# Kernel tuning notes

Hardware: AMD Instinct MI355X
Metric: run time of the kernel (lower is better)

## Reference

```python
import jax, jax.numpy as jnp
import numpy as np

FACTOR = 5

def setup_inputs() -> dict:
    key = jax.random.key(0)
    k1, k2, k3, k4 = jax.random.split(key, 4)
    B, L, H, D = 4, 4096, 8, 64
    sample_k = min(FACTOR * int(np.ceil(np.log(L))), L)  # 45
    queries = jax.random.normal(k1, (B, L, H, D), jnp.float32)
    keys = jax.random.normal(k2, (B, L, H, D), jnp.float32)
    values = jax.random.normal(k3, (B, L, H, D), jnp.float32)
    # torch.randint(L_K, (L_Q, sample_k)) hoisted here for determinism
    index_sample = jax.random.randint(k4, (L, sample_k), 0, L, dtype=jnp.int32)
    return {"queries": queries, "keys": keys, "values": values,
            "index_sample": index_sample}


def reference(queries, keys, values, index_sample):
    B, L_Q, H, D = queries.shape
    L_K = keys.shape[1]
    # [B,L,H,D] -> [B,H,L,D]
    Q = jnp.transpose(queries, (0, 2, 1, 3))
    K = jnp.transpose(keys, (0, 2, 1, 3))
    V = jnp.transpose(values, (0, 2, 1, 3))

    u = min(FACTOR * int(np.ceil(np.log(L_Q))), L_Q)  # n_top queries

    # --- _prob_QK: sampled QK, sparsity measure, top-u query selection ---
    # K_sample[b,h,q,s,:] = K[b,h,index_sample[q,s],:]
    K_sample = K[:, :, index_sample, :]                        # [B,H,L_Q,Sk,D]
    Q_K_sample = jnp.einsum('bhqd,bhqsd->bhqs', Q, K_sample)   # [B,H,L_Q,Sk]
    M = Q_K_sample.max(axis=-1) - Q_K_sample.sum(axis=-1) / L_K
    _, M_top = jax.lax.top_k(M, u)                             # [B,H,u]

    Q_reduce = jnp.take_along_axis(Q, M_top[..., None], axis=2)  # [B,H,u,D]
    scale = 1.0 / np.sqrt(D).astype(np.float32)
    scores = jnp.einsum('bhud,bhkd->bhuk', Q_reduce, K) * scale  # [B,H,u,L_K]

    # --- masked causal attention on the selected rows (mask_flag=True) ---
    # ProbMask: triu(1) rows gathered at M_top -> mask where col > query pos
    causal_mask = M_top[..., None] < jnp.arange(L_K)             # [B,H,u,L_K]
    scores = jnp.where(causal_mask, -jnp.inf, scores)
    attn = jax.nn.softmax(scores, axis=-1)

    # --- initial context (masked => cumsum of V), scatter top-u updates ---
    context = jnp.cumsum(V, axis=2)                              # [B,H,L_Q,D]
    update = jnp.einsum('bhuk,bhkd->bhud', attn, V)              # [B,H,u,D]
    b_idx = jnp.arange(B)[:, None, None]
    h_idx = jnp.arange(H)[None, :, None]
    context = context.at[b_idx, h_idx, M_top].set(update)
    return context  # [B,H,L_Q,D]
```

## Files before the change

kernel.cpp:

```cpp
#include <hip/hip_runtime.h>
#include <float.h>
#include <math.h>

#define B_ 4
#define L_ 4096
#define H_ 8
#define D_ 64
#define S_ 45
#define KC_ 16
#define KCH_ 256
#define SCALE 0.125f

typedef __attribute__((ext_vector_type(8))) short short8;
typedef __attribute__((ext_vector_type(4))) float float4v;

__device__ __forceinline__ ushort f2bf(float x) {
  unsigned u = __float_as_uint(x);
  return (ushort)((u + 0x7FFFu + ((u >> 16) & 1u)) >> 16);
}

__device__ __forceinline__ int swz_us(int row, int col_b, int rowb, int m) {
  int slot = (col_b >> 4) ^ (row & m);
  return row * (rowb >> 1) + (slot << 3) + ((col_b & 15) >> 1);
}

__global__ __launch_bounds__(256) void kA(
    const float* __restrict__ Q, const float* __restrict__ K,
    const float* __restrict__ V, const int* __restrict__ idxs,
    float* __restrict__ M, float* __restrict__ cs)
{
  int blk = blockIdx.x;
  int grp = blk / 136, within = blk % 136;
  int tid = threadIdx.x;
  int w = tid >> 6, lane = tid & 63;

  if (within >= 128) {
    if (grp >= 64) return;
    int cblk = grp * 8 + (within - 128);
    int bh = cblk >> 4, cg = cblk & 15;
    int b = bh >> 3, h = bh & 7;
    int t = lane & 15, rg = lane >> 4;
    int c = cg * 4 + w;
    int l0 = c * 64;
    const float4* V4 = (const float4*)V;
    float4 acc = make_float4(0.f, 0.f, 0.f, 0.f);
    for (int step = 0; step < 16; ++step) {
      int l = l0 + step * 4 + rg;
      float4 v = V4[((size_t)(b * L_ + l) * H_ + h) * 16 + t];
      acc.x += v.x; acc.y += v.y; acc.z += v.z; acc.w += v.w;
    }
    acc.x += __shfl_xor(acc.x, 16, 64); acc.y += __shfl_xor(acc.y, 16, 64);
    acc.z += __shfl_xor(acc.z, 16, 64); acc.w += __shfl_xor(acc.w, 16, 64);
    acc.x += __shfl_xor(acc.x, 32, 64); acc.y += __shfl_xor(acc.y, 32, 64);
    acc.z += __shfl_xor(acc.z, 32, 64); acc.w += __shfl_xor(acc.w, 32, 64);
    if (rg == 0)
      ((float4*)cs)[((size_t)bh * 64 + c) * 16 + t] = acc;
    return;
  }

  int kblk = grp * 128 + within;
  int phase = kblk >> 13;
  int pblk = kblk & 8191;
  int g = pblk & 7;
  int b = (g >> 2) + phase * 2;
  int hq = g & 3;
  int chunk = pblk >> 3;
  int l = chunk * 4 + w;
  int t31 = lane & 31;
  int half = lane >> 5;

  const float4* qp =
      (const float4*)(Q + ((size_t)(b * L_ + l) * H_ + hq * 2) * D_);
  float4 qv = qp[t31];

  int s = lane < S_ ? lane : S_ - 1;
  int idxall = idxs[l * S_ + s];

  float vmax = -FLT_MAX, vsum = 0.f;
  #pragma unroll
  for (int c = 0; c < 3; ++c) {
    int kidx[6];
    #pragma unroll
    for (int jj = 0; jj < 6; ++jj)
      kidx[jj] = __shfl(idxall, (c * 6 + jj) * 2 + half, 64);
    float4 kv[6];
    #pragma unroll
    for (int jj = 0; jj < 6; ++jj)
      kv[jj] = ((const float4*)(K +
          ((size_t)(b * L_ + kidx[jj]) * H_ + hq * 2) * D_))[t31];
    #pragma unroll
    for (int jj = 0; jj < 6; ++jj) {
      float p = qv.x * kv[jj].x;
      p = fmaf(qv.y, kv[jj].y, p);
      p = fmaf(qv.z, kv[jj].z, p);
      p = fmaf(qv.w, kv[jj].w, p);
      p += __shfl_xor(p, 1, 64);
      p += __shfl_xor(p, 2, 64);
      p += __shfl_xor(p, 4, 64);
      p += __shfl_xor(p, 8, 64);
      vmax = fmaxf(vmax, p);
      vsum += p;
    }
  }
  {
    int kidx[5];
    #pragma unroll
    for (int jj = 0; jj < 5; ++jj) {
      int s2 = (18 + jj) * 2 + half;
      kidx[jj] = __shfl(idxall, s2 > 44 ? 44 : s2, 64);
    }
    float4 kv[5];
    #pragma unroll
    for (int jj = 0; jj < 5; ++jj)
      kv[jj] = ((const float4*)(K +
          ((size_t)(b * L_ + kidx[jj]) * H_ + hq * 2) * D_))[t31];
    #pragma unroll
    for (int jj = 0; jj < 5; ++jj) {
      float p = qv.x * kv[jj].x;
      p = fmaf(qv.y, kv[jj].y, p);
      p = fmaf(qv.z, kv[jj].z, p);
      p = fmaf(qv.w, kv[jj].w, p);
      p += __shfl_xor(p, 1, 64);
      p += __shfl_xor(p, 2, 64);
      p += __shfl_xor(p, 4, 64);
      p += __shfl_xor(p, 8, 64);
      bool dup = (jj == 4) && (half == 1);
      vmax = fmaxf(vmax, p);
      if (!dup) vsum += p;
    }
  }
  vmax = fmaxf(vmax, __shfl_xor(vmax, 32, 64));
  vsum += __shfl_xor(vsum, 32, 64);
  if ((lane & 15) == 0 && half == 0) {
    int h = hq * 2 + (lane >> 4);
    M[(size_t)(b * H_ + h) * L_ + l] = vmax - vsum * (1.0f / L_);
  }
}

__device__ __forceinline__ unsigned ordf(float f) {
  unsigned u = __float_as_uint(f);
  return (u & 0x80000000u) ? ~u : (u | 0x80000000u);
}

__global__ __launch_bounds__(256) void kB(
    const float* __restrict__ M, int* __restrict__ mtop, float* __restrict__ cs)
{
  int blk = blockIdx.x;
  int tid = threadIdx.x;
  if (blk >= 32) {
    int g = (blk - 32) * 256 + tid;
    int bh = g >> 6, d = g & 63;
    float v[64];
    #pragma unroll
    for (int c = 0; c < 64; ++c) v[c] = cs[((size_t)bh * 64 + c) * D_ + d];
    float run = 0.f;
    #pragma unroll
    for (int c = 0; c < 64; ++c) {
      float a = v[c];
      cs[((size_t)bh * 64 + c) * D_ + d] = run;
      run += a;
    }
    return;
  }
  __shared__ unsigned long long cand[4][S_];
  int bh = blk;
  int w = tid >> 6, lane = tid & 63;
  const float* Mp = M + (size_t)bh * L_;
  unsigned long long key[16];
  #pragma unroll
  for (int j = 0; j < 16; ++j) {
    int gi = w * 1024 + j * 64 + lane;
    key[j] = ((unsigned long long)ordf(Mp[gi]) << 32) | (unsigned)(~gi);
  }
  for (int it = 0; it < S_; ++it) {
    unsigned long long loc = key[0];
    #pragma unroll
    for (int j = 1; j < 16; ++j) loc = key[j] > loc ? key[j] : loc;
    unsigned long long best = loc;
    #pragma unroll
    for (int m = 32; m >= 1; m >>= 1) {
      unsigned long long o = __shfl_xor(best, m, 64);
      best = o > best ? o : best;
    }
    if (loc == best) {
      #pragma unroll
      for (int j = 0; j < 16; ++j) if (key[j] == best) key[j] = 0ull;
    }
    if (lane == 0) cand[w][it] = best;
  }
  __syncthreads();
  if (w == 0) {
    unsigned long long k2[3];
    #pragma unroll
    for (int j = 0; j < 3; ++j) {
      int c = j * 64 + lane;
      k2[j] = (c < 4 * S_) ? cand[c / S_][c % S_] : 0ull;
    }
    for (int it = 0; it < S_; ++it) {
      unsigned long long loc = k2[0];
      loc = k2[1] > loc ? k2[1] : loc;
      loc = k2[2] > loc ? k2[2] : loc;
      unsigned long long best = loc;
      #pragma unroll
      for (int m = 32; m >= 1; m >>= 1) {
        unsigned long long o = __shfl_xor(best, m, 64);
        best = o > best ? o : best;
      }
      if (loc == best) {
        #pragma unroll
        for (int j = 0; j < 3; ++j) if (k2[j] == best) k2[j] = 0ull;
      }
      if (lane == 0) mtop[bh * S_ + it] = (int)(~(unsigned)(best & 0xFFFFFFFFu));
    }
  }
}

__global__ __launch_bounds__(256) void kATT(
    const float* __restrict__ Q, const float* __restrict__ K,
    const float* __restrict__ V, const int* __restrict__ mtop,
    float* __restrict__ lpart, float* __restrict__ updp)
{
  __shared__ __align__(16) ushort Ks[256 * 64];
  __shared__ __align__(16) ushort Qs[48 * 64];
  __shared__ __align__(16) ushort Ps[48 * 256];
  __shared__ float lred[4][48];
  __shared__ int   cut[48];

  int blk = blockIdx.x;
  int kc = blk >> 5;
  int r5 = blk & 31;
  int bh = ((r5 & 7) << 2) | (r5 >> 3);
  int b = bh >> 3, h = bh & 7;
  int tid = threadIdx.x;
  int w = tid >> 6, lane = tid & 63;
  int l15 = lane & 15, l4 = lane >> 4;

  if (tid < 48) cut[tid] = (tid < S_) ? mtop[bh * S_ + tid] : -1;
  __syncthreads();

  {
    const float4* kp =
        (const float4*)(K + ((size_t)(b * L_ + kc * KCH_ + tid) * H_ + h) * D_);
    #pragma unroll
    for (int c = 0; c < 8; ++c) {
      float4 a = kp[2 * c], bb = kp[2 * c + 1];
      uint4 pk;
      pk.x = f2bf(a.x) | ((unsigned)f2bf(a.y) << 16);
      pk.y = f2bf(a.z) | ((unsigned)f2bf(a.w) << 16);
      pk.z = f2bf(bb.x) | ((unsigned)f2bf(bb.y) << 16);
      pk.w = f2bf(bb.z) | ((unsigned)f2bf(bb.w) << 16);
      *(uint4*)&Ks[swz_us(tid, c * 16, 128, 7)] = pk;
    }
  }
  for (int i = tid; i < 48 * 8; i += 256) {
    int row = i >> 3, c = i & 7;
    uint4 pk = make_uint4(0, 0, 0, 0);
    if (row < S_) {
      const float4* qp =
          (const float4*)(Q + ((size_t)(b * L_ + cut[row]) * H_ + h) * D_);
      float4 a = qp[2 * c], bb = qp[2 * c + 1];
      pk.x = f2bf(a.x) | ((unsigned)f2bf(a.y) << 16);
      pk.y = f2bf(a.z) | ((unsigned)f2bf(a.w) << 16);
      pk.z = f2bf(bb.x) | ((unsigned)f2bf(bb.y) << 16);
      pk.w = f2bf(bb.z) | ((unsigned)f2bf(bb.w) << 16);
    }
    *(uint4*)&Qs[swz_us(row, c * 16, 128, 7)] = pk;
  }
  __syncthreads();

  float4v accS[3][4];
  #pragma unroll
  for (int mt = 0; mt < 3; ++mt)
    #pragma unroll
    for (int nt = 0; nt < 4; ++nt)
      accS[mt][nt] = (float4v){0.f, 0.f, 0.f, 0.f};
  #pragma unroll
  for (int ks = 0; ks < 2; ++ks) {
    short8 afr[3];
    #pragma unroll
    for (int mt = 0; mt < 3; ++mt)
      afr[mt] = *(const short8*)&Qs[swz_us(mt * 16 + l15, ks * 64 + l4 * 16, 128, 7)];
    #pragma unroll
    for (int nt = 0; nt < 4; ++nt) {
      short8 bfr = *(const short8*)
          &Ks[swz_us(w * 64 + nt * 16 + l15, ks * 64 + l4 * 16, 128, 7)];
      #pragma unroll
      for (int mt = 0; mt < 3; ++mt)
        accS[mt][nt] = __builtin_amdgcn_mfma_f32_16x16x32_bf16(
            afr[mt], bfr, accS[mt][nt], 0, 0, 0);
    }
  }

  #pragma unroll
  for (int mt = 0; mt < 3; ++mt) {
    #pragma unroll
    for (int j = 0; j < 4; ++j) {
      int row = mt * 16 + l4 * 4 + j;
      int ct = cut[row];
      float rs = 0.f;
      #pragma unroll
      for (int nt = 0; nt < 4; ++nt) {
        int col = w * 64 + nt * 16 + l15;
        int kg = kc * KCH_ + col;
        float e = (kg <= ct) ? __expf(accS[mt][nt][j] * SCALE) : 0.f;
        rs += e;
        Ps[swz_us(row, col * 2, 512, 15)] = f2bf(e);
      }
      rs += __shfl_xor(rs, 1, 64);
      rs += __shfl_xor(rs, 2, 64);
      rs += __shfl_xor(rs, 4, 64);
      rs += __shfl_xor(rs, 8, 64);
      if (l15 == 0) lred[w][row] = rs;
    }
  }
  __syncthreads();

  if (tid < S_)
    lpart[((size_t)(bh * KC_ + kc)) * S_ + tid] =
        lred[0][tid] + lred[1][tid] + lred[2][tid] + lred[3][tid];

  {
    const float4* vp =
        (const float4*)(V + ((size_t)(b * L_ + kc * KCH_ + tid) * H_ + h) * D_);
    #pragma unroll
    for (int c = 0; c < 16; ++c) {
      float4 v = vp[c];
      int d0 = c * 4;
      Ks[swz_us(d0 + 0, tid * 2, 512, 15)] = f2bf(v.x);
      Ks[swz_us(d0 + 1, tid * 2, 512, 15)] = f2bf(v.y);
      Ks[swz_us(d0 + 2, tid * 2, 512, 15)] = f2bf(v.z);
      Ks[swz_us(d0 + 3, tid * 2, 512, 15)] = f2bf(v.w);
    }
  }
  __syncthreads();

  float4v accU[3];
  #pragma unroll
  for (int i = 0; i < 3; ++i) accU[i] = (float4v){0.f, 0.f, 0.f, 0.f};
  #pragma unroll
  for (int ks = 0; ks < 8; ++ks) {
    #pragma unroll
    for (int i = 0; i < 3; ++i) {
      int pi = w * 3 + i, mt = pi >> 2, nt = pi & 3;
      short8 afr = *(const short8*)
          &Ps[swz_us(mt * 16 + l15, ks * 64 + l4 * 16, 512, 15)];
      short8 bfr = *(const short8*)
          &Ks[swz_us(nt * 16 + l15, ks * 64 + l4 * 16, 512, 15)];
      accU[i] = __builtin_amdgcn_mfma_f32_16x16x32_bf16(afr, bfr, accU[i], 0, 0, 0);
    }
  }
  float* up = updp + ((size_t)(bh * KC_ + kc)) * (S_ * D_);
  #pragma unroll
  for (int i = 0; i < 3; ++i) {
    int pi = w * 3 + i, mt = pi >> 2, nt = pi & 3;
    #pragma unroll
    for (int j = 0; j < 4; ++j) {
      int row = mt * 16 + l4 * 4 + j;
      if (row < S_) up[row * D_ + nt * 16 + l15] = accU[i][j];
    }
  }
}

__global__ __launch_bounds__(256) void kWD(
    const float* __restrict__ V, const float* __restrict__ cs,
    const float* __restrict__ lpart, const float* __restrict__ updp,
    const int* __restrict__ mtop, float* __restrict__ out)
{
  int blk = blockIdx.x;
  int tid = threadIdx.x;

  if (blk >= 512) {
    __shared__ float linv[S_];
    __shared__ int   mt[S_];
    int bh = blk - 512;
    if (tid < S_) {
      float l = 0.f;
      for (int kc = 0; kc < KC_; ++kc) l += lpart[(size_t)(bh * KC_ + kc) * S_ + tid];
      linv[tid] = 1.0f / l;
      mt[tid] = mtop[bh * S_ + tid];
    }
    __syncthreads();
    for (int i = tid; i < S_ * D_; i += 256) {
      int r = i >> 6, d = i & 63;
      float u = 0.f;
      for (int kc = 0; kc < KC_; ++kc)
        u += updp[((size_t)(bh * KC_ + kc)) * (S_ * D_) + i];
      out[((size_t)bh * L_ + mt[r]) * D_ + d] = u * linv[r];
    }
    return;
  }

  __shared__ unsigned bits[8];
  int bh = blk >> 4, cg = blk & 15;
  int base = cg * 256;
  if (tid < 8) bits[tid] = 0u;
  __syncthreads();
  if (tid < S_) {
    int r = mtop[bh * S_ + tid] - base;
    if ((unsigned)r < 256u) atomicOr(&bits[r >> 5], 1u << (r & 31));
  }
  __syncthreads();

  int b = bh >> 3, h = bh & 7;
  int w = tid >> 6, lane = tid & 63;
  int t = lane & 15, rg = lane >> 4;
  int c = cg * 4 + w;
  int l0 = c * 64;
  const float4* V4 = (const float4*)V;
  float4* O4 = (float4*)out;
  float4 carry = ((const float4*)cs)[((size_t)bh * 64 + c) * 16 + t];
  for (int step = 0; step < 16; ++step) {
    int l = l0 + step * 4 + rg;
    float4 v = V4[((size_t)(b * L_ + l) * H_ + h) * 16 + t];
    float4 u;
    u.x = __shfl_up(v.x, 16, 64); u.y = __shfl_up(v.y, 16, 64);
    u.z = __shfl_up(v.z, 16, 64); u.w = __shfl_up(v.w, 16, 64);
    if (rg >= 1) { v.x += u.x; v.y += u.y; v.z += u.z; v.w += u.w; }
    u.x = __shfl_up(v.x, 32, 64); u.y = __shfl_up(v.y, 32, 64);
    u.z = __shfl_up(v.z, 32, 64); u.w = __shfl_up(v.w, 32, 64);
    if (rg >= 2) { v.x += u.x; v.y += u.y; v.z += u.z; v.w += u.w; }
    int wl = l - base;
    if (!((bits[wl >> 5] >> (wl & 31)) & 1u)) {
      float4 o;
      o.x = carry.x + v.x; o.y = carry.y + v.y;
      o.z = carry.z + v.z; o.w = carry.w + v.w;
      O4[((size_t)bh * L_ + l) * 16 + t] = o;
    }
    carry.x += __shfl(v.x, 48 + t, 64); carry.y += __shfl(v.y, 48 + t, 64);
    carry.z += __shfl(v.z, 48 + t, 64); carry.w += __shfl(v.w, 48 + t, 64);
  }
}

extern "C" void kernel_launch(void* const* d_in, const int* in_sizes, int n_in,
                              void* d_out, int out_size, void* d_ws, size_t ws_size,
                              hipStream_t stream) {
  const float* Q = (const float*)d_in[0];
  const float* K = (const float*)d_in[1];
  const float* V = (const float*)d_in[2];
  const int*   I = (const int*)d_in[3];
  float* out = (float*)d_out;
  float* ws = (float*)d_ws;

  float* M     = ws;
  float* cs    = ws + 131072;
  float* lpart = ws + 262144;
  float* updp  = ws + 262144 + 23040;
  int*   mtop  = (int*)(ws + 262144 + 23040 + 1474560);

  kA<<<128 * 136, 256, 0, stream>>>(Q, K, V, I, M, cs);
  kB<<<40, 256, 0, stream>>>(M, mtop, cs);
  kATT<<<B_ * H_ * KC_, 256, 0, stream>>>(Q, K, V, mtop, lpart, updp);
  kWD<<<544, 256, 0, stream>>>(V, cs, lpart, updp, mtop, out);
}
```

Measured before the change: 174.9 us.

## Merge top-k, attention and writeback into one cooperative kernel with grid syncs

New measurement: 380.4 us. 117% more time.

```diff
diff --git a/kernel.cpp b/kernel.cpp
--- a/kernel.cpp
+++ b/kernel.cpp
@@ -1,6 +1,9 @@
 #include <hip/hip_runtime.h>
+#include <hip/hip_cooperative_groups.h>
 #include <float.h>
 #include <math.h>
+
+namespace cg = cooperative_groups;
 
 #define B_ 4
 #define L_ 4096
@@ -22,6 +25,11 @@
 __device__ __forceinline__ int swz_us(int row, int col_b, int rowb, int m) {
   int slot = (col_b >> 4) ^ (row & m);
   return row * (rowb >> 1) + (slot << 3) + ((col_b & 15) >> 1);
+}
+
+__device__ __forceinline__ unsigned ordf(float f) {
+  unsigned u = __float_as_uint(f);
+  return (u & 0x80000000u) ? ~u : (u | 0x80000000u);
 }
 
 __global__ __launch_bounds__(256) void kA(
@@ -137,88 +145,12 @@
   }
 }
 
-__device__ __forceinline__ unsigned ordf(float f) {
-  unsigned u = __float_as_uint(f);
-  return (u & 0x80000000u) ? ~u : (u | 0x80000000u);
-}
-
-__global__ __launch_bounds__(256) void kB(
-    const float* __restrict__ M, int* __restrict__ mtop, float* __restrict__ cs)
-{
-  int blk = blockIdx.x;
-  int tid = threadIdx.x;
-  if (blk >= 32) {
-    int g = (blk - 32) * 256 + tid;
-    int bh = g >> 6, d = g & 63;
-    float v[64];
-    #pragma unroll
-    for (int c = 0; c < 64; ++c) v[c] = cs[((size_t)bh * 64 + c) * D_ + d];
-    float run = 0.f;
-    #pragma unroll
-    for (int c = 0; c < 64; ++c) {
-      float a = v[c];
-      cs[((size_t)bh * 64 + c) * D_ + d] = run;
-      run += a;
-    }
-    return;
-  }
-  __shared__ unsigned long long cand[4][S_];
-  int bh = blk;
-  int w = tid >> 6, lane = tid & 63;
-  const float* Mp = M + (size_t)bh * L_;
-  unsigned long long key[16];
-  #pragma unroll
-  for (int j = 0; j < 16; ++j) {
-    int gi = w * 1024 + j * 64 + lane;
-    key[j] = ((unsigned long long)ordf(Mp[gi]) << 32) | (unsigned)(~gi);
-  }
-  for (int it = 0; it < S_; ++it) {
-    unsigned long long loc = key[0];
-    #pragma unroll
-    for (int j = 1; j < 16; ++j) loc = key[j] > loc ? key[j] : loc;
-    unsigned long long best = loc;
-    #pragma unroll
-    for (int m = 32; m >= 1; m >>= 1) {
-      unsigned long long o = __shfl_xor(best, m, 64);
-      best = o > best ? o : best;
-    }
-    if (loc == best) {
-      #pragma unroll
-      for (int j = 0; j < 16; ++j) if (key[j] == best) key[j] = 0ull;
-    }
-    if (lane == 0) cand[w][it] = best;
-  }
-  __syncthreads();
-  if (w == 0) {
-    unsigned long long k2[3];
-    #pragma unroll
-    for (int j = 0; j < 3; ++j) {
-      int c = j * 64 + lane;
-      k2[j] = (c < 4 * S_) ? cand[c / S_][c % S_] : 0ull;
-    }
-    for (int it = 0; it < S_; ++it) {
-      unsigned long long loc = k2[0];
-      loc = k2[1] > loc ? k2[1] : loc;
-      loc = k2[2] > loc ? k2[2] : loc;
-      unsigned long long best = loc;
-      #pragma unroll
-      for (int m = 32; m >= 1; m >>= 1) {
-        unsigned long long o = __shfl_xor(best, m, 64);
-        best = o > best ? o : best;
-      }
-      if (loc == best) {
-        #pragma unroll
-        for (int j = 0; j < 3; ++j) if (k2[j] == best) k2[j] = 0ull;
-      }
-      if (lane == 0) mtop[bh * S_ + it] = (int)(~(unsigned)(best & 0xFFFFFFFFu));
-    }
-  }
-}
-
-__global__ __launch_bounds__(256) void kATT(
+__global__ __launch_bounds__(256) void kT(
     const float* __restrict__ Q, const float* __restrict__ K,
-    const float* __restrict__ V, const int* __restrict__ mtop,
-    float* __restrict__ lpart, float* __restrict__ updp)
+    const float* __restrict__ V, const float* __restrict__ M,
+    float* __restrict__ cs, int* __restrict__ mtop,
+    float* __restrict__ lpart, float* __restrict__ updp,
+    float* __restrict__ out, int phase)
 {
   __shared__ __align__(16) ushort Ks[256 * 64];
   __shared__ __align__(16) ushort Qs[48 * 64];
@@ -227,207 +159,286 @@
   __shared__ int   cut[48];
 
   int blk = blockIdx.x;
+  int tid = threadIdx.x;
+  int w = tid >> 6, lane = tid & 63;
+  bool coop = (phase == 0);
+
   int kc = blk >> 5;
   int r5 = blk & 31;
-  int bh = ((r5 & 7) << 2) | (r5 >> 3);
-  int b = bh >> 3, h = bh & 7;
-  int tid = threadIdx.x;
-  int w = tid >> 6, lane = tid & 63;
-  int l15 = lane & 15, l4 = lane >> 4;
-
-  if (tid < 48) cut[tid] = (tid < S_) ? mtop[bh * S_ + tid] : -1;
-  __syncthreads();
-
-  {
-    const float4* kp =
-        (const float4*)(K + ((size_t)(b * L_ + kc * KCH_ + tid) * H_ + h) * D_);
-    #pragma unroll
-    for (int c = 0; c < 8; ++c) {
-      float4 a = kp[2 * c], bb = kp[2 * c + 1];
-      uint4 pk;
-      pk.x = f2bf(a.x) | ((unsigned)f2bf(a.y) << 16);
-      pk.y = f2bf(a.z) | ((unsigned)f2bf(a.w) << 16);
-      pk.z = f2bf(bb.x) | ((unsigned)f2bf(bb.y) << 16);
-      pk.w = f2bf(bb.z) | ((unsigned)f2bf(bb.w) << 16);
-      *(uint4*)&Ks[swz_us(tid, c * 16, 128, 7)] = pk;
-    }
-  }
-  for (int i = tid; i < 48 * 8; i += 256) {
-    int row = i >> 3, c = i & 7;
-    uint4 pk = make_uint4(0, 0, 0, 0);
-    if (row < S_) {
-      const float4* qp =
-          (const float4*)(Q + ((size_t)(b * L_ + cut[row]) * H_ + h) * D_);
-      float4 a = qp[2 * c], bb = qp[2 * c + 1];
-      pk.x = f2bf(a.x) | ((unsigned)f2bf(a.y) << 16);
-      pk.y = f2bf(a.z) | ((unsigned)f2bf(a.w) << 16);
-      pk.z = f2bf(bb.x) | ((unsigned)f2bf(bb.y) << 16);
-      pk.w = f2bf(bb.z) | ((unsigned)f2bf(bb.w) << 16);
-    }
-    *(uint4*)&Qs[swz_us(row, c * 16, 128, 7)] = pk;
-  }
-  __syncthreads();
-
-  float4v accS[3][4];
-  #pragma unroll
-  for (int mt = 0; mt < 3; ++mt)
-    #pragma unroll
-    for (int nt = 0; nt < 4; ++nt)
-      accS[mt][nt] = (float4v){0.f, 0.f, 0.f, 0.f};
-  #pragma unroll
-  for (int ks = 0; ks < 2; ++ks) {
-    short8 afr[3];
+  int bh_att = ((r5 & 7) << 2) | (r5 >> 3);
+  int b_att = bh_att >> 3, h_att = bh_att & 7;
+
+  if (coop || phase == 1) {
+    if (blk < 32) {
+      unsigned long long (*cand)[S_] = (unsigned long long (*)[S_])Ps;
+      int bh = blk;
+      const float* Mp = M + (size_t)bh * L_;
+      unsigned long long key[16];
+      #pragma unroll
+      for (int j = 0; j < 16; ++j) {
+        int gi = w * 1024 + j * 64 + lane;
+        key[j] = ((unsigned long long)ordf(Mp[gi]) << 32) | (unsigned)(~gi);
+      }
+      for (int it = 0; it < S_; ++it) {
+        unsigned long long loc = key[0];
+        #pragma unroll
+        for (int j = 1; j < 16; ++j) loc = key[j] > loc ? key[j] : loc;
+        unsigned long long best = loc;
+        #pragma unroll
+        for (int m = 32; m >= 1; m >>= 1) {
+          unsigned long long o = __shfl_xor(best, m, 64);
+          best = o > best ? o : best;
+        }
+        if (loc == best) {
+          #pragma unroll
+          for (int j = 0; j < 16; ++j) if (key[j] == best) key[j] = 0ull;
+        }
+        if (lane == 0) cand[w][it] = best;
+      }
+      __syncthreads();
+      if (w == 0) {
+        unsigned long long k2[3];
+        #pragma unroll
+        for (int j = 0; j < 3; ++j) {
+          int c = j * 64 + lane;
+          k2[j] = (c < 4 * S_) ? cand[c / S_][c % S_] : 0ull;
+        }
+        for (int it = 0; it < S_; ++it) {
+          unsigned long long loc = k2[0];
+          loc = k2[1] > loc ? k2[1] : loc;
+          loc = k2[2] > loc ? k2[2] : loc;
+          unsigned long long best = loc;
+          #pragma unroll
+          for (int m = 32; m >= 1; m >>= 1) {
+            unsigned long long o = __shfl_xor(best, m, 64);
+            best = o > best ? o : best;
+          }
+          if (loc == best) {
+            #pragma unroll
+            for (int j = 0; j < 3; ++j) if (k2[j] == best) k2[j] = 0ull;
+          }
+          if (lane == 0) mtop[bh * S_ + it] = (int)(~(unsigned)(best & 0xFFFFFFFFu));
+        }
+      }
+    } else if (blk < 40) {
+      int g = (blk - 32) * 256 + tid;
+      int bh = g >> 6, d = g & 63;
+      float v[64];
+      #pragma unroll
+      for (int c = 0; c < 64; ++c) v[c] = cs[((size_t)bh * 64 + c) * D_ + d];
+      float run = 0.f;
+      #pragma unroll
+      for (int c = 0; c < 64; ++c) {
+        float a = v[c];
+        cs[((size_t)bh * 64 + c) * D_ + d] = run;
+        run += a;
+      }
+    } else if (coop) {
+      const float4* kp =
+          (const float4*)(K + ((size_t)(b_att * L_ + kc * KCH_ + tid) * H_ + h_att) * D_);
+      #pragma unroll
+      for (int c = 0; c < 8; ++c) {
+        float4 a = kp[2 * c], bb = kp[2 * c + 1];
+        uint4 pk;
+        pk.x = f2bf(a.x) | ((unsigned)f2bf(a.y) << 16);
+        pk.y = f2bf(a.z) | ((unsigned)f2bf(a.w) << 16);
+        pk.z = f2bf(bb.x) | ((unsigned)f2bf(bb.y) << 16);
+        pk.w = f2bf(bb.z) | ((unsigned)f2bf(bb.w) << 16);
+        *(uint4*)&Ks[swz_us(tid, c * 16, 128, 7)] = pk;
+      }
+    }
+  }
+  if (coop) { __threadfence(); cg::this_grid().sync(); }
+
+  if (coop || phase == 2) {
+    if (!coop || blk < 40) {
+      const float4* kp =
+          (const float4*)(K + ((size_t)(b_att * L_ + kc * KCH_ + tid) * H_ + h_att) * D_);
+      #pragma unroll
+      for (int c = 0; c < 8; ++c) {
+        float4 a = kp[2 * c], bb = kp[2 * c + 1];
+        uint4 pk;
+        pk.x = f2bf(a.x) | ((unsigned)f2bf(a.y) << 16);
+        pk.y = f2bf(a.z) | ((unsigned)f2bf(a.w) << 16);
+        pk.z = f2bf(bb.x) | ((unsigned)f2bf(bb.y) << 16);
+        pk.w = f2bf(bb.z) | ((unsigned)f2bf(bb.w) << 16);
+        *(uint4*)&Ks[swz_us(tid, c * 16, 128, 7)] = pk;
+      }
+    }
+    if (tid < 48) cut[tid] = (tid < S_) ? mtop[bh_att * S_ + tid] : -1;
+    __syncthreads();
+    for (int i = tid; i < 48 * 8; i += 256) {
+      int row = i >> 3, c = i & 7;
+      uint4 pk = make_uint4(0, 0, 0, 0);
+      if (row < S_) {
+        const float4* qp =
+            (const float4*)(Q + ((size_t)(b_att * L_ + cut[row]) * H_ + h_att) * D_);
+        float4 a = qp[2 * c], bb = qp[2 * c + 1];
+        pk.x = f2bf(a.x) | ((unsigned)f2bf(a.y) << 16);
+        pk.y = f2bf(a.z) | ((unsigned)f2bf(a.w) << 16);
+        pk.z = f2bf(bb.x) | ((unsigned)f2bf(bb.y) << 16);
+        pk.w = f2bf(bb.z) | ((unsigned)f2bf(bb.w) << 16);
+      }
+      *(uint4*)&Qs[swz_us(row, c * 16, 128, 7)] = pk;
+    }
+    __syncthreads();
+
+    int l15 = lane & 15, l4 = lane >> 4;
+    float4v accS[3][4];
     #pragma unroll
     for (int mt = 0; mt < 3; ++mt)
-      afr[mt] = *(const short8*)&Qs[swz_us(mt * 16 + l15, ks * 64 + l4 * 16, 128, 7)];
-    #pragma unroll
-    for (int nt = 0; nt < 4; ++nt) {
-      short8 bfr = *(const short8*)
-          &Ks[swz_us(w * 64 + nt * 16 + l15, ks * 64 + l4 * 16, 128, 7)];
+      #pragma unroll
+      for (int nt = 0; nt < 4; ++nt)
+        accS[mt][nt] = (float4v){0.f, 0.f, 0.f, 0.f};
+    #pragma unroll
+    for (int ks = 0; ks < 2; ++ks) {
+      short8 afr[3];
       #pragma unroll
       for (int mt = 0; mt < 3; ++mt)
-        accS[mt][nt] = __builtin_amdgcn_mfma_f32_16x16x32_bf16(
-            afr[mt], bfr, accS[mt][nt], 0, 0, 0);
-    }
-  }
-
-  #pragma unroll
-  for (int mt = 0; mt < 3; ++mt) {
-    #pragma unroll
-    for (int j = 0; j < 4; ++j) {
-      int row = mt * 16 + l4 * 4 + j;
-      int ct = cut[row];
-      float rs = 0.f;
+        afr[mt] = *(const short8*)&Qs[swz_us(mt * 16 + l15, ks * 64 + l4 * 16, 128, 7)];
       #pragma unroll
       for (int nt = 0; nt < 4; ++nt) {
-        int col = w * 64 + nt * 16 + l15;
-        int kg = kc * KCH_ + col;
-        float e = (kg <= ct) ? __expf(accS[mt][nt][j] * SCALE) : 0.f;
-        rs += e;
-        Ps[swz_us(row, col * 2, 512, 15)] = f2bf(e);
-      }
-      rs += __shfl_xor(rs, 1, 64);
-      rs += __shfl_xor(rs, 2, 64);
-      rs += __shfl_xor(rs, 4, 64);
-      rs += __shfl_xor(rs, 8, 64);
-      if (l15 == 0) lred[w][row] = rs;
-    }
-  }
-  __syncthreads();
-
-  if (tid < S_)
-    lpart[((size_t)(bh * KC_ + kc)) * S_ + tid] =
-        lred[0][tid] + lred[1][tid] + lred[2][tid] + lred[3][tid];
-
-  {
-    const float4* vp =
-        (const float4*)(V + ((size_t)(b * L_ + kc * KCH_ + tid) * H_ + h) * D_);
-    #pragma unroll
-    for (int c = 0; c < 16; ++c) {
-      float4 v = vp[c];
-      int d0 = c * 4;
-      Ks[swz_us(d0 + 0, tid * 2, 512, 15)] = f2bf(v.x);
-      Ks[swz_us(d0 + 1, tid * 2, 512, 15)] = f2bf(v.y);
-      Ks[swz_us(d0 + 2, tid * 2, 512, 15)] = f2bf(v.z);
-      Ks[swz_us(d0 + 3, tid * 2, 512, 15)] = f2bf(v.w);
-    }
-  }
-  __syncthreads();
-
-  float4v accU[3];
-  #pragma unroll
-  for (int i = 0; i < 3; ++i) accU[i] = (float4v){0.f, 0.f, 0.f, 0.f};
-  #pragma unroll
-  for (int ks = 0; ks < 8; ++ks) {
+        short8 bfr = *(const short8*)
+            &Ks[swz_us(w * 64 + nt * 16 + l15, ks * 64 + l4 * 16, 128, 7)];
+        #pragma unroll
+        for (int mt = 0; mt < 3; ++mt)
+          accS[mt][nt] = __builtin_amdgcn_mfma_f32_16x16x32_bf16(
+              afr[mt], bfr, accS[mt][nt], 0, 0, 0);
+      }
+    }
+
+    #pragma unroll
+    for (int mt = 0; mt < 3; ++mt) {
+      #pragma unroll
+      for (int j = 0; j < 4; ++j) {
+        int row = mt * 16 + l4 * 4 + j;
+        int ct = cut[row];
+        float rs = 0.f;
+        #pragma unroll
+        for (int nt = 0; nt < 4; ++nt) {
+          int col = w * 64 + nt * 16 + l15;
+          int kg = kc * KCH_ + col;
+          float e = (kg <= ct) ? __expf(accS[mt][nt][j] * SCALE) : 0.f;
+          rs += e;
+          Ps[swz_us(row, col * 2, 512, 15)] = f2bf(e);
+        }
+        rs += __shfl_xor(rs, 1, 64);
+        rs += __shfl_xor(rs, 2, 64);
+        rs += __shfl_xor(rs, 4, 64);
+        rs += __shfl_xor(rs, 8, 64);
+        if (l15 == 0) lred[w][row] = rs;
+      }
+    }
+    __syncthreads();
+
+    if (tid < S_)
+      lpart[((size_t)(bh_att * KC_ + kc)) * S_ + tid] =
+          lred[0][tid] + lred[1][tid] + lred[2][tid] + lred[3][tid];
+
+    {
+      const float4* vp =
+          (const float4*)(V + ((size_t)(b_att * L_ + kc * KCH_ + tid) * H_ + h_att) * D_);
+      #pragma unroll
+      for (int c = 0; c < 16; ++c) {
+        float4 v = vp[c];
+        int d0 = c * 4;
+        Ks[swz_us(d0 + 0, tid * 2, 512, 15)] = f2bf(v.x);
+        Ks[swz_us(d0 + 1, tid * 2, 512, 15)] = f2bf(v.y);
+        Ks[swz_us(d0 + 2, tid * 2, 512, 15)] = f2bf(v.z);
+        Ks[swz_us(d0 + 3, tid * 2, 512, 15)] = f2bf(v.w);
+      }
+    }
+    __syncthreads();
+
+    float4v accU[3];
+    #pragma unroll
+    for (int i = 0; i < 3; ++i) accU[i] = (float4v){0.f, 0.f, 0.f, 0.f};
+    #pragma unroll
+    for (int ks = 0; ks < 8; ++ks) {
+      #pragma unroll
+      for (int i = 0; i < 3; ++i) {
+        int pi = w * 3 + i, mt = pi >> 2, nt = pi & 3;
+        short8 afr = *(const short8*)
+            &Ps[swz_us(mt * 16 + l15, ks * 64 + l4 * 16, 512, 15)];
+        short8 bfr = *(const short8*)
+            &Ks[swz_us(nt * 16 + l15, ks * 64 + l4 * 16, 512, 15)];
+        accU[i] = __builtin_amdgcn_mfma_f32_16x16x32_bf16(afr, bfr, accU[i], 0, 0, 0);
+      }
+    }
+    float* up = updp + ((size_t)(bh_att * KC_ + kc)) * (S_ * D_);
     #pragma unroll
     for (int i = 0; i < 3; ++i) {
       int pi = w * 3 + i, mt = pi >> 2, nt = pi & 3;
-      short8 afr = *(const short8*)
-          &Ps[swz_us(mt * 16 + l15, ks * 64 + l4 * 16, 512, 15)];
-      short8 bfr = *(const short8*)
-          &Ks[swz_us(nt * 16 + l15, ks * 64 + l4 * 16, 512, 15)];
-      accU[i] = __builtin_amdgcn_mfma_f32_16x16x32_bf16(afr, bfr, accU[i], 0, 0, 0);
-    }
-  }
-  float* up = updp + ((size_t)(bh * KC_ + kc)) * (S_ * D_);
-  #pragma unroll
-  for (int i = 0; i < 3; ++i) {
-    int pi = w * 3 + i, mt = pi >> 2, nt = pi & 3;
-    #pragma unroll
-    for (int j = 0; j < 4; ++j) {
-      int row = mt * 16 + l4 * 4 + j;
-      if (row < S_) up[row * D_ + nt * 16 + l15] = accU[i][j];
-    }
-  }
-}
-
-__global__ __launch_bounds__(256) void kWD(
-    const float* __restrict__ V, const float* __restrict__ cs,
-    const float* __restrict__ lpart, const float* __restrict__ updp,
-    const int* __restrict__ mtop, float* __restrict__ out)
-{
-  int blk = blockIdx.x;
-  int tid = threadIdx.x;
-
-  if (blk >= 512) {
-    __shared__ float linv[S_];
-    __shared__ int   mt[S_];
-    int bh = blk - 512;
+      #pragma unroll
+      for (int j = 0; j < 4; ++j) {
+        int row = mt * 16 + l4 * 4 + j;
+        if (row < S_) up[row * D_ + nt * 16 + l15] = accU[i][j];
+      }
+    }
+  }
+  if (coop) { __threadfence(); cg::this_grid().sync(); }
+
+  if (coop || phase == 3) {
+    unsigned* bits = (unsigned*)cut;
+    int bh = blk >> 4, cg2 = blk & 15;
+    int base = cg2 * 256;
+    if (tid < 8) bits[tid] = 0u;
+    __syncthreads();
     if (tid < S_) {
-      float l = 0.f;
-      for (int kc = 0; kc < KC_; ++kc) l += lpart[(size_t)(bh * KC_ + kc) * S_ + tid];
-      linv[tid] = 1.0f / l;
-      mt[tid] = mtop[bh * S_ + tid];
-    }
-    __syncthreads();
-    for (int i = tid; i < S_ * D_; i += 256) {
-      int r = i >> 6, d = i & 63;
-      float u = 0.f;
-      for (int kc = 0; kc < KC_; ++kc)
-        u += updp[((size_t)(bh * KC_ + kc)) * (S_ * D_) + i];
-      out[((size_t)bh * L_ + mt[r]) * D_ + d] = u * linv[r];
-    }
-    return;
-  }
-
-  __shared__ unsigned bits[8];
-  int bh = blk >> 4, cg = blk & 15;
-  int base = cg * 256;
-  if (tid < 8) bits[tid] = 0u;
-  __syncthreads();
-  if (tid < S_) {
-    int r = mtop[bh * S_ + tid] - base;
-    if ((unsigned)r < 256u) atomicOr(&bits[r >> 5], 1u << (r & 31));
-  }
-  __syncthreads();
-
-  int b = bh >> 3, h = bh & 7;
-  int w = tid >> 6, lane = tid & 63;
-  int t = lane & 15, rg = lane >> 4;
-  int c = cg * 4 + w;
-  int l0 = c * 64;
-  const float4* V4 = (const float4*)V;
-  float4* O4 = (float4*)out;
-  float4 carry = ((const float4*)cs)[((size_t)bh * 64 + c) * 16 + t];
-  for (int step = 0; step < 16; ++step) {
-    int l = l0 + step * 4 + rg;
-    float4 v = V4[((size_t)(b * L_ + l) * H_ + h) * 16 + t];
-    float4 u;
-    u.x = __shfl_up(v.x, 16, 64); u.y = __shfl_up(v.y, 16, 64);
-    u.z = __shfl_up(v.z, 16, 64); u.w = __shfl_up(v.w, 16, 64);
-    if (rg >= 1) { v.x += u.x; v.y += u.y; v.z += u.z; v.w += u.w; }
-    u.x = __shfl_up(v.x, 32, 64); u.y = __shfl_up(v.y, 32, 64);
-    u.z = __shfl_up(v.z, 32, 64); u.w = __shfl_up(v.w, 32, 64);
-    if (rg >= 2) { v.x += u.x; v.y += u.y; v.z += u.z; v.w += u.w; }
-    int wl = l - base;
-    if (!((bits[wl >> 5] >> (wl & 31)) & 1u)) {
-      float4 o;
-      o.x = carry.x + v.x; o.y = carry.y + v.y;
-      o.z = carry.z + v.z; o.w = carry.w + v.w;
-      O4[((size_t)bh * L_ + l) * 16 + t] = o;
-    }
-    carry.x += __shfl(v.x, 48 + t, 64); carry.y += __shfl(v.y, 48 + t, 64);
-    carry.z += __shfl(v.z, 48 + t, 64); carry.w += __shfl(v.w, 48 + t, 64);
+      int r = mtop[bh * S_ + tid] - base;
+      if ((unsigned)r < 256u) atomicOr(&bits[r >> 5], 1u << (r & 31));
+    }
+    __syncthreads();
+
+    int b = bh >> 3, h = bh & 7;
+    int t = lane & 15, rg = lane >> 4;
+    int c = cg2 * 4 + w;
+    int l0 = c * 64;
+    const float4* V4 = (const float4*)V;
+    float4* O4 = (float4*)out;
+    float4 carry = ((const float4*)cs)[((size_t)bh * 64 + c) * 16 + t];
+    for (int step = 0; step < 16; ++step) {
+      int l = l0 + step * 4 + rg;
+      float4 v = V4[((size_t)(b * L_ + l) * H_ + h) * 16 + t];
+      float4 u;
+      u.x = __shfl_up(v.x, 16, 64); u.y = __shfl_up(v.y, 16, 64);
+      u.z = __shfl_up(v.z, 16, 64); u.w = __shfl_up(v.w, 16, 64);
+      if (rg >= 1) { v.x += u.x; v.y += u.y; v.z += u.z; v.w += u.w; }
+      u.x = __shfl_up(v.x, 32, 64); u.y = __shfl_up(v.y, 32, 64);
+      u.z = __shfl_up(v.z, 32, 64); u.w = __shfl_up(v.w, 32, 64);
+      if (rg >= 2) { v.x += u.x; v.y += u.y; v.z += u.z; v.w += u.w; }
+      int wl = l - base;
+      if (!((bits[wl >> 5] >> (wl & 31)) & 1u)) {
+        float4 o;
+        o.x = carry.x + v.x; o.y = carry.y + v.y;
+        o.z = carry.z + v.z; o.w = carry.w + v.w;
+        O4[((size_t)bh * L_ + l) * 16 + t] = o;
+      }
+      carry.x += __shfl(v.x, 48 + t, 64); carry.y += __shfl(v.y, 48 + t, 64);
+      carry.z += __shfl(v.z, 48 + t, 64); carry.w += __shfl(v.w, 48 + t, 64);
+    }
+
+    if (blk < 32) {
+      float* linv = (float*)lred;
+      int*   mt2  = (int*)(lred) + 64;
+      int bhf = blk;
+      __syncthreads();
+      if (tid < S_) {
+        float l = 0.f;
+        for (int kcc = 0; kcc < KC_; ++kcc)
+          l += lpart[(size_t)(bhf * KC_ + kcc) * S_ + tid];
+        linv[tid] = 1.0f / l;
+        mt2[tid] = mtop[bhf * S_ + tid];
+      }
+      __syncthreads();
+      for (int i = tid; i < S_ * D_; i += 256) {
+        int r = i >> 6, d = i & 63;
+        float u = 0.f;
+        for (int kcc = 0; kcc < KC_; ++kcc)
+          u += updp[((size_t)(bhf * KC_ + kcc)) * (S_ * D_) + i];
+        out[((size_t)bhf * L_ + mt2[r]) * D_ + d] = u * linv[r];
+      }
+    }
   }
 }
 
@@ -448,7 +459,17 @@
   int*   mtop  = (int*)(ws + 262144 + 23040 + 1474560);
 
   kA<<<128 * 136, 256, 0, stream>>>(Q, K, V, I, M, cs);
-  kB<<<40, 256, 0, stream>>>(M, mtop, cs);
-  kATT<<<B_ * H_ * KC_, 256, 0, stream>>>(Q, K, V, mtop, lpart, updp);
-  kWD<<<544, 256, 0, stream>>>(V, cs, lpart, updp, mtop, out);
-}
+
+  int ph0 = 0;
+  void* args[] = {(void*)&Q, (void*)&K, (void*)&V, (void*)&M, (void*)&cs,
+                  (void*)&mtop, (void*)&lpart, (void*)&updp, (void*)&out,
+                  (void*)&ph0};
+  hipError_t e = hipLaunchCooperativeKernel((void*)kT, dim3(512), dim3(256),
+                                            args, 0, stream);
+  if (e != hipSuccess) {
+    (void)hipGetLastError();
+    kT<<<40, 256, 0, stream>>>(Q, K, V, M, cs, mtop, lpart, updp, out, 1);
+    kT<<<512, 256, 0, stream>>>(Q, K, V, M, cs, mtop, lpart, updp, out, 2);
+    kT<<<512, 256, 0, stream>>>(Q, K, V, M, cs, mtop, lpart, updp, out, 3);
+  }
+}
```

## Merge cumsum writeback into attention kernel and prefetch V into registers

Applied to the files above, without the earlier changes.

Result: slower. 187.9 us (+7.4%).

```diff
diff --git a/kernel.cpp b/kernel.cpp
--- a/kernel.cpp
+++ b/kernel.cpp
@@ -22,6 +22,11 @@
 __device__ __forceinline__ int swz_us(int row, int col_b, int rowb, int m) {
   int slot = (col_b >> 4) ^ (row & m);
   return row * (rowb >> 1) + (slot << 3) + ((col_b & 15) >> 1);
+}
+
+__device__ __forceinline__ unsigned ordf(float f) {
+  unsigned u = __float_as_uint(f);
+  return (u & 0x80000000u) ? ~u : (u | 0x80000000u);
 }
 
 __global__ __launch_bounds__(256) void kA(
@@ -135,11 +140,6 @@
     int h = hq * 2 + (lane >> 4);
     M[(size_t)(b * H_ + h) * L_ + l] = vmax - vsum * (1.0f / L_);
   }
-}
-
-__device__ __forceinline__ unsigned ordf(float f) {
-  unsigned u = __float_as_uint(f);
-  return (u & 0x80000000u) ? ~u : (u | 0x80000000u);
 }
 
 __global__ __launch_bounds__(256) void kB(
@@ -215,25 +215,80 @@
   }
 }
 
-__global__ __launch_bounds__(256) void kATT(
+__global__ __launch_bounds__(256) void kAW(
     const float* __restrict__ Q, const float* __restrict__ K,
-    const float* __restrict__ V, const int* __restrict__ mtop,
-    float* __restrict__ lpart, float* __restrict__ updp)
+    const float* __restrict__ V, const float* __restrict__ cs,
+    const int* __restrict__ mtop, float* __restrict__ lpart,
+    float* __restrict__ updp, float* __restrict__ out)
 {
   __shared__ __align__(16) ushort Ks[256 * 64];
   __shared__ __align__(16) ushort Qs[48 * 64];
   __shared__ __align__(16) ushort Ps[48 * 256];
   __shared__ float lred[4][48];
   __shared__ int   cut[48];
+  __shared__ unsigned bits[8];
 
   int blk = blockIdx.x;
-  int kc = blk >> 5;
-  int r5 = blk & 31;
+  int grp = blk >> 4, within = blk & 15;
+  int tid = threadIdx.x;
+  int w = tid >> 6, lane = tid & 63;
+
+  if (within >= 8) {
+    int wblk = grp * 8 + (within - 8);
+    int bh = wblk >> 4, cg2 = wblk & 15;
+    int base = cg2 * 256;
+    if (tid < 8) bits[tid] = 0u;
+    __syncthreads();
+    if (tid < S_) {
+      int r = mtop[bh * S_ + tid] - base;
+      if ((unsigned)r < 256u) atomicOr(&bits[r >> 5], 1u << (r & 31));
+    }
+    __syncthreads();
+
+    int b = bh >> 3, h = bh & 7;
+    int t = lane & 15, rg = lane >> 4;
+    int c = cg2 * 4 + w;
+    int l0 = c * 64;
+    const float4* V4 = (const float4*)V;
+    float4* O4 = (float4*)out;
+    float4 carry = ((const float4*)cs)[((size_t)bh * 64 + c) * 16 + t];
+    for (int step = 0; step < 16; ++step) {
+      int l = l0 + step * 4 + rg;
+      float4 v = V4[((size_t)(b * L_ + l) * H_ + h) * 16 + t];
+      float4 u;
+      u.x = __shfl_up(v.x, 16, 64); u.y = __shfl_up(v.y, 16, 64);
+      u.z = __shfl_up(v.z, 16, 64); u.w = __shfl_up(v.w, 16, 64);
+      if (rg >= 1) { v.x += u.x; v.y += u.y; v.z += u.z; v.w += u.w; }
+      u.x = __shfl_up(v.x, 32, 64); u.y = __shfl_up(v.y, 32, 64);
+      u.z = __shfl_up(v.z, 32, 64); u.w = __shfl_up(v.w, 32, 64);
+      if (rg >= 2) { v.x += u.x; v.y += u.y; v.z += u.z; v.w += u.w; }
+      int wl = l - base;
+      if (!((bits[wl >> 5] >> (wl & 31)) & 1u)) {
+        float4 o;
+        o.x = carry.x + v.x; o.y = carry.y + v.y;
+        o.z = carry.z + v.z; o.w = carry.w + v.w;
+        O4[((size_t)bh * L_ + l) * 16 + t] = o;
+      }
+      carry.x += __shfl(v.x, 48 + t, 64); carry.y += __shfl(v.y, 48 + t, 64);
+      carry.z += __shfl(v.z, 48 + t, 64); carry.w += __shfl(v.w, 48 + t, 64);
+    }
+    return;
+  }
+
+  int ablk = grp * 8 + within;
+  int kc = ablk >> 5;
+  int r5 = ablk & 31;
   int bh = ((r5 & 7) << 2) | (r5 >> 3);
   int b = bh >> 3, h = bh & 7;
-  int tid = threadIdx.x;
-  int w = tid >> 6, lane = tid & 63;
   int l15 = lane & 15, l4 = lane >> 4;
+
+  float4 vreg[16];
+  {
+    const float4* vp =
+        (const float4*)(V + ((size_t)(b * L_ + kc * KCH_ + tid) * H_ + h) * D_);
+    #pragma unroll
+    for (int c = 0; c < 16; ++c) vreg[c] = vp[c];
+  }
 
   if (tid < 48) cut[tid] = (tid < S_) ? mtop[bh * S_ + tid] : -1;
   __syncthreads();
@@ -319,18 +374,14 @@
     lpart[((size_t)(bh * KC_ + kc)) * S_ + tid] =
         lred[0][tid] + lred[1][tid] + lred[2][tid] + lred[3][tid];
 
-  {
-    const float4* vp =
-        (const float4*)(V + ((size_t)(b * L_ + kc * KCH_ + tid) * H_ + h) * D_);
-    #pragma unroll
-    for (int c = 0; c < 16; ++c) {
-      float4 v = vp[c];
-      int d0 = c * 4;
-      Ks[swz_us(d0 + 0, tid * 2, 512, 15)] = f2bf(v.x);
-      Ks[swz_us(d0 + 1, tid * 2, 512, 15)] = f2bf(v.y);
-      Ks[swz_us(d0 + 2, tid * 2, 512, 15)] = f2bf(v.z);
-      Ks[swz_us(d0 + 3, tid * 2, 512, 15)] = f2bf(v.w);
-    }
+  #pragma unroll
+  for (int c = 0; c < 16; ++c) {
+    float4 v = vreg[c];
+    int d0 = c * 4;
+    Ks[swz_us(d0 + 0, tid * 2, 512, 15)] = f2bf(v.x);
+    Ks[swz_us(d0 + 1, tid * 2, 512, 15)] = f2bf(v.y);
+    Ks[swz_us(d0 + 2, tid * 2, 512, 15)] = f2bf(v.z);
+    Ks[swz_us(d0 + 3, tid * 2, 512, 15)] = f2bf(v.w);
   }
   __syncthreads();
 
@@ -361,73 +412,26 @@
   }
 }
 
-__global__ __launch_bounds__(256) void kWD(
-    const float* __restrict__ V, const float* __restrict__ cs,
+__global__ __launch_bounds__(256) void kFin(
     const float* __restrict__ lpart, const float* __restrict__ updp,
     const int* __restrict__ mtop, float* __restrict__ out)
 {
-  int blk = blockIdx.x;
+  __shared__ float linv[S_];
+  __shared__ int   mt[S_];
+  int bh = blockIdx.x;
   int tid = threadIdx.x;
-
-  if (blk >= 512) {
-    __shared__ float linv[S_];
-    __shared__ int   mt[S_];
-    int bh = blk - 512;
-    if (tid < S_) {
-      float l = 0.f;
-      for (int kc = 0; kc < KC_; ++kc) l += lpart[(size_t)(bh * KC_ + kc) * S_ + tid];
-      linv[tid] = 1.0f / l;
-      mt[tid] = mtop[bh * S_ + tid];
-    }
-    __syncthreads();
-    for (int i = tid; i < S_ * D_; i += 256) {
-      int r = i >> 6, d = i & 63;
-      float u = 0.f;
-      for (int kc = 0; kc < KC_; ++kc)
-        u += updp[((size_t)(bh * KC_ + kc)) * (S_ * D_) + i];
-      out[((size_t)bh * L_ + mt[r]) * D_ + d] = u * linv[r];
-    }
-    return;
-  }
-
-  __shared__ unsigned bits[8];
-  int bh = blk >> 4, cg = blk & 15;
-  int base = cg * 256;
-  if (tid < 8) bits[tid] = 0u;
-  __syncthreads();
   if (tid < S_) {
-    int r = mtop[bh * S_ + tid] - base;
-    if ((unsigned)r < 256u) atomicOr(&bits[r >> 5], 1u << (r & 31));
-  }
-  __syncthreads();
-
-  int b = bh >> 3, h = bh & 7;
-  int w = tid >> 6, lane = tid & 63;
-  int t = lane & 15, rg = lane >> 4;
-  int c = cg * 4 + w;
-  int l0 = c * 64;
-  const float4* V4 = (const float4*)V;
-  float4* O4 = (float4*)out;
-  float4 carry = ((const float4*)cs)[((size_t)bh * 64 + c) * 16 + t];
-  for (int step = 0; step < 16; ++step) {
-    int l = l0 + step * 4 + rg;
-    float4 v = V4[((size_t)(b * L_ + l) * H_ + h) * 16 + t];
-    float4 u;
-    u.x = __shfl_up(v.x, 16, 64); u.y = __shfl_up(v.y, 16, 64);
-    u.z = __shfl_up(v.z, 16, 64); u.w = __shfl_up(v.w, 16, 64);
-    if (rg >= 1) { v.x += u.x; v.y += u.y; v.z += u.z; v.w += u.w; }
-    u.x = __shfl_up(v.x, 32, 64); u.y = __shfl_up(v.y, 32, 64);
-    u.z = __shfl_up(v.z, 32, 64); u.w = __shfl_up(v.w, 32, 64);
-    if (rg >= 2) { v.x += u.x; v.y += u.y; v.z += u.z; v.w += u.w; }
-    int wl = l - base;
-    if (!((bits[wl >> 5] >> (wl & 31)) & 1u)) {
-      float4 o;
-      o.x = carry.x + v.x; o.y = carry.y + v.y;
-      o.z = carry.z + v.z; o.w = carry.w + v.w;
-      O4[((size_t)bh * L_ + l) * 16 + t] = o;
-    }
-    carry.x += __shfl(v.x, 48 + t, 64); carry.y += __shfl(v.y, 48 + t, 64);
-    carry.z += __shfl(v.z, 48 + t, 64); carry.w += __shfl(v.w, 48 + t, 64);
+    float l = 0.f;
+    for (int kc = 0; kc < KC_; ++kc) l += lpart[(size_t)(bh * KC_ + kc) * S_ + tid];
+    linv[tid] = 1.0f / l;
+    mt[tid] = mtop[bh * S_ + tid];
+  }
+  __syncthreads();
+  for (int i = tid; i < S_ * D_; i += 256) {
+    int r = i >> 6, d = i & 63;
+    float u = 0.f;
+    for (int kc = 0; kc < KC_; ++kc) u += updp[((size_t)(bh * KC_ + kc)) * (S_ * D_) + i];
+    out[((size_t)bh * L_ + mt[r]) * D_ + d] = u * linv[r];
   }
 }
 
@@ -449,6 +453,6 @@
 
   kA<<<128 * 136, 256, 0, stream>>>(Q, K, V, I, M, cs);
   kB<<<40, 256, 0, stream>>>(M, mtop, cs);
-  kATT<<<B_ * H_ * KC_, 256, 0, stream>>>(Q, K, V, mtop, lpart, updp);
-  kWD<<<544, 256, 0, stream>>>(V, cs, lpart, updp, mtop, out);
-}
+  kAW<<<64 * 16, 256, 0, stream>>>(Q, K, V, cs, mtop, lpart, updp, out);
+  kFin<<<B_ * H_, 256, 0, stream>>>(lpart, updp, mtop, out);
+}
```
